# Kernel optimization log

Measured on AMD Instinct MI355X. Metric: run time of the kernel, lower is better.

Reference implementation:

```python
import jax, jax.numpy as jnp
import numpy as np

B, S, D, H = 2, 2048, 2048, 16
HD = D // H
F = 4 * D
EPS = 1e-8


def _layernorm(x, g, b):
    m = jnp.mean(x, axis=-1, keepdims=True)
    v = jnp.mean((x - m) ** 2, axis=-1, keepdims=True)
    return (x - m) / jnp.sqrt(v + EPS) * g + b


def setup_inputs() -> dict:
    key = jax.random.key(0)
    ks = jax.random.split(key, 12)

    def lin(k, fan_in, fan_out):
        # torch Linear init ~ U(-1/sqrt(fan_in), 1/sqrt(fan_in)); stored as [in, out]
        lim = 1.0 / np.sqrt(fan_in)
        kw, kb = jax.random.split(k)
        w = jax.random.uniform(kw, (fan_in, fan_out), jnp.float32, -lim, lim)
        b = jax.random.uniform(kb, (fan_out,), jnp.float32, -lim, lim)
        return w, b

    x = jax.random.normal(ks[0], (B, S, D), jnp.float32)
    wq, bq = lin(ks[1], D, D)
    wk, bk = lin(ks[2], D, D)
    wv, bv = lin(ks[3], D, D)
    wo, bo = lin(ks[4], D, D)
    wu, bu = lin(ks[5], D, F)
    wd, bd = lin(ks[6], F, D)
    g1 = jnp.ones((D,), jnp.float32)
    b1 = jnp.zeros((D,), jnp.float32)
    g2 = jnp.ones((D,), jnp.float32)
    b2 = jnp.zeros((D,), jnp.float32)
    return dict(x=x, wq=wq, bq=bq, wk=wk, bk=bk, wv=wv, bv=bv, wo=wo, bo=bo,
                g1=g1, b1=b1, wu=wu, bu=bu, wd=wd, bd=bd, g2=g2, b2=b2)


def reference(x, wq, bq, wk, bk, wv, bv, wo, bo, g1, b1, wu, bu, wd, bd, g2, b2):
    b, s, d = x.shape
    # QKV projections -> [b, H, s, HD]
    q = (x @ wq + bq).reshape(b, s, H, HD).transpose(0, 2, 1, 3)
    k = (x @ wk + bk).reshape(b, s, H, HD).transpose(0, 2, 1, 3)
    v = (x @ wv + bv).reshape(b, s, H, HD).transpose(0, 2, 1, 3)
    # scaled dot-product with causal mask filled at -1e9 (matches masked_fill)
    scores = jnp.einsum('bhqd,bhkd->bhqk', q, k) / np.sqrt(HD).astype(np.float32)
    causal = jnp.tril(jnp.ones((s, s), bool))
    scores = jnp.where(causal, scores, jnp.float32(-1e9))
    attn = jax.nn.softmax(scores, axis=-1)  # dropout is identity (eval / rate=0)
    o = jnp.einsum('bhqk,bhkd->bhqd', attn, v)
    o = o.transpose(0, 2, 1, 3).reshape(b, s, d)
    o = o @ wo + bo
    x = _layernorm(x + o, g1, b1)
    # FFN with exact (erf) GELU, residual, LN
    h = jax.nn.gelu(x @ wu + bu, approximate=False)
    h = h @ wd + bd
    return _layernorm(x + h, g2, b2)
```

## Files before the change

### kernel.cpp

```cpp
#include <hip/hip_runtime.h>
#include <hip/hip_bf16.h>
#include <math.h>

#define DEV __device__ __forceinline__

typedef __bf16 bf16x8 __attribute__((ext_vector_type(8)));
typedef float f32x4 __attribute__((ext_vector_type(4)));
typedef unsigned short ushort_t;
typedef ushort_t us8 __attribute__((ext_vector_type(8)));
typedef ushort_t us4 __attribute__((ext_vector_type(4)));

DEV float bf2f(ushort_t u) {
    unsigned v = ((unsigned)u) << 16;
    float f; __builtin_memcpy(&f, &v, 4); return f;
}
DEV ushort_t f2bf(float f) {
    unsigned u; __builtin_memcpy(&u, &f, 4);
    u += 0x7fffu + ((u >> 16) & 1);
    return (ushort_t)(u >> 16);
}

DEV void gload16(const void* g, void* l) {
    __builtin_amdgcn_global_load_lds(
        (const __attribute__((address_space(1))) void*)g,
        (__attribute__((address_space(3))) void*)l, 16, 0, 0);
}

__global__ __launch_bounds__(256) void fill_kernel(float* out, long n, float v) {
    long i = (long)blockIdx.x * blockDim.x + threadIdx.x;
    if (i < n) out[i] = v;
}

__global__ __launch_bounds__(256) void cast_bf16_kernel(
    const float* __restrict__ in, ushort_t* __restrict__ out, long n)
{
    long i = ((long)blockIdx.x * blockDim.x + threadIdx.x) * 4;
    if (i >= n) return;
    float4 v = *(const float4*)(in + i);
    us4 o = { f2bf(v.x), f2bf(v.y), f2bf(v.z), f2bf(v.w) };
    *(us4*)(out + i) = o;
}

__global__ __launch_bounds__(256) void transpose_bf16_kernel(
    const float* __restrict__ in, ushort_t* __restrict__ out, int R, int C)
{
    __shared__ float tile[32][33];
    int c0 = blockIdx.x * 32, r0 = blockIdx.y * 32;
    int tx = threadIdx.x & 31, ty = threadIdx.x >> 5;
#pragma unroll
    for (int j = 0; j < 4; ++j) {
        int r = ty + j * 8;
        tile[r][tx] = in[(long)(r0 + r) * C + (c0 + tx)];
    }
    __syncthreads();
#pragma unroll
    for (int j = 0; j < 4; ++j) {
        int r = ty + j * 8;
        out[(long)(c0 + r) * R + (r0 + tx)] = f2bf(tile[tx][r]);
    }
}

__global__ __launch_bounds__(256) void gemm_bt_kernel(
    const ushort_t* __restrict__ A, const ushort_t* __restrict__ Bt,
    const float* __restrict__ bias, ushort_t* __restrict__ C,
    int M, int N, int K, int act)
{
    __shared__ __align__(16) ushort_t lA[128 * 64];
    __shared__ __align__(16) ushort_t lB[128 * 64];
    const int t = threadIdx.x;
    const int w = t >> 6, l = t & 63;
    const int wr = w >> 1, wc = w & 1;
    const long m0 = (long)blockIdx.x * 128;
    const long n0 = (long)blockIdx.y * 128;

    const int sr = l >> 3;
    const int scol = (l & 7) * 16;

    f32x4 acc[4][4];
    f32x4 zf = {0.f, 0.f, 0.f, 0.f};
#pragma unroll
    for (int i = 0; i < 4; ++i)
#pragma unroll
        for (int j = 0; j < 4; ++j) acc[i][j] = zf;

    const char* Ab = (const char*)(A + m0 * K);
    const char* Bb = (const char*)(Bt + n0 * K);
    char* lAc = (char*)lA;
    char* lBc = (char*)lB;

    for (int k0 = 0; k0 < K; k0 += 64) {
        __syncthreads();
#pragma unroll
        for (int c = 0; c < 4; ++c) {
            int row = (w * 4 + c) * 8 + sr;
            int src = scol ^ ((row & 7) << 4);
            gload16(Ab + (long)row * (K * 2) + (long)k0 * 2 + src, lAc + (w * 4 + c) * 1024);
            gload16(Bb + (long)row * (K * 2) + (long)k0 * 2 + src, lBc + (w * 4 + c) * 1024);
        }
        __syncthreads();
#pragma unroll
        for (int ks = 0; ks < 2; ++ks) {
            bf16x8 af[4], bfr[4];
#pragma unroll
            for (int i = 0; i < 4; ++i) {
                int row = wr * 64 + i * 16 + (l & 15);
                int cb = (ks * 64 + (l >> 4) * 16) ^ ((row & 7) << 4);
                af[i] = *(const bf16x8*)(lAc + row * 128 + cb);
            }
#pragma unroll
            for (int j = 0; j < 4; ++j) {
                int row = wc * 64 + j * 16 + (l & 15);
                int cb = (ks * 64 + (l >> 4) * 16) ^ ((row & 7) << 4);
                bfr[j] = *(const bf16x8*)(lBc + row * 128 + cb);
            }
#pragma unroll
            for (int i = 0; i < 4; ++i)
#pragma unroll
                for (int j = 0; j < 4; ++j)
                    acc[i][j] = __builtin_amdgcn_mfma_f32_16x16x32_bf16(af[i], bfr[j], acc[i][j], 0, 0, 0);
        }
    }

#pragma unroll
    for (int j = 0; j < 4; ++j) {
        int col = (int)n0 + wc * 64 + j * 16 + (l & 15);
        float bv = bias[col];
#pragma unroll
        for (int i = 0; i < 4; ++i) {
            long rowb = m0 + wr * 64 + i * 16 + (l >> 4) * 4;
#pragma unroll
            for (int r = 0; r < 4; ++r) {
                float v2 = acc[i][j][r] + bv;
                if (act == 1) v2 = 0.5f * v2 * (1.f + erff(v2 * 0.70710678118654752440f));
                C[(rowb + r) * (long)N + col] = f2bf(v2);
            }
        }
    }
}

__global__ __launch_bounds__(512, 4) void attn_kernel(
    const ushort_t* __restrict__ qkv, ushort_t* __restrict__ o)
{
    __shared__ __align__(16) ushort_t lK[2 * 64 * 128];
    __shared__ __align__(16) ushort_t lVT[128 * 72];
    __shared__ __align__(16) ushort_t lP[8 * 16 * 64];

    const int t = threadIdx.x, w = t >> 6, l = t & 63;
    const int qblk = blockIdx.x, bh = blockIdx.y;
    const int b = bh >> 4, h = bh & 15;
    const int q0 = qblk * 128 + w * 16;
    const long base = (long)b * 2048 * 6144 + (long)h * 128;
    const ushort_t* Kg = qkv + base + 2048;
    const ushort_t* Vg = qkv + base + 4096;
    char* lKc = (char*)lK;

    const ushort_t* qrow = qkv + base + (long)(q0 + (l & 15)) * 6144;
    bf16x8 qf[4];
#pragma unroll
    for (int hb = 0; hb < 4; ++hb)
        qf[hb] = *(const bf16x8*)(qrow + hb * 32 + (l >> 4) * 8);

    f32x4 accO[8];
    f32x4 zf = {0.f, 0.f, 0.f, 0.f};
#pragma unroll
    for (int i = 0; i < 8; ++i) accO[i] = zf;
    float m_r[4] = {-1e30f, -1e30f, -1e30f, -1e30f};
    float l_r[4] = {0.f, 0.f, 0.f, 0.f};

    const int nt = (qblk * 128 + 128) >> 6;
    const float scale = 0.08838834764831845f;

    const int kvp = t & 31;
    const int d0 = (t >> 5) * 8;
    us8 va, vb;

    auto stageK = [&](int kt, int buf) {
#pragma unroll
        for (int i = 0; i < 2; ++i) {
            int c = w * 2 + i;
            int row = c * 4 + (l >> 4);
            int src = ((l & 15) * 16) ^ ((row & 7) << 4);
            gload16((const char*)(Kg + (long)(kt * 64 + row) * 6144) + src,
                    lKc + buf * 16384 + c * 1024);
        }
    };
    auto loadV = [&](int kt) {
        const ushort_t* vr = Vg + (long)(kt * 64 + kvp * 2) * 6144 + d0;
        va = *(const us8*)vr;
        vb = *(const us8*)(vr + 6144);
    };
    auto writeVT = [&]() {
#pragma unroll
        for (int j = 0; j < 8; ++j) {
            unsigned pk = (unsigned)va[j] | ((unsigned)vb[j] << 16);
            *(unsigned*)(lVT + (d0 + j) * 72 + kvp * 2) = pk;
        }
    };

    stageK(0, 0);
    loadV(0);
    asm volatile("s_waitcnt vmcnt(0)" ::: "memory");
    writeVT();
    __syncthreads();

    for (int t0 = 0; t0 < nt; ++t0) {
        const int cur = t0 & 1;
        const bool more = (t0 + 1 < nt);
        if (more) { stageK(t0 + 1, cur ^ 1); loadV(t0 + 1); }

        const int kv0 = t0 * 64;
        if (kv0 <= q0 + 15) {
            f32x4 sc[4];
#pragma unroll
            for (int kvs = 0; kvs < 4; ++kvs) {
                sc[kvs] = zf;
                int row = kvs * 16 + (l & 15);
#pragma unroll
                for (int hb = 0; hb < 4; ++hb) {
                    int cb = (hb * 64 + (l >> 4) * 16) ^ ((row & 7) << 4);
                    bf16x8 kf = *(const bf16x8*)(lKc + cur * 16384 + row * 256 + cb);
                    sc[kvs] = __builtin_amdgcn_mfma_f32_16x16x32_bf16(qf[hb], kf, sc[kvs], 0, 0, 0);
                }
            }
#pragma unroll
            for (int r = 0; r < 4; ++r) {
                int qg = q0 + (l >> 4) * 4 + r;
                float s[4];
#pragma unroll
                for (int kvs = 0; kvs < 4; ++kvs) {
                    s[kvs] = sc[kvs][r] * scale;
                    if (kv0 + kvs * 16 + (l & 15) > qg) s[kvs] = -1e30f;
                }
                float pm = fmaxf(fmaxf(s[0], s[1]), fmaxf(s[2], s[3]));
                pm = fmaxf(pm, __shfl_xor(pm, 1));
                pm = fmaxf(pm, __shfl_xor(pm, 2));
                pm = fmaxf(pm, __shfl_xor(pm, 4));
                pm = fmaxf(pm, __shfl_xor(pm, 8));
                float mn = fmaxf(m_r[r], pm);
                float p[4], ps = 0.f;
#pragma unroll
                for (int kvs = 0; kvs < 4; ++kvs) { p[kvs] = __expf(s[kvs] - mn); ps += p[kvs]; }
                ps += __shfl_xor(ps, 1);
                ps += __shfl_xor(ps, 2);
                ps += __shfl_xor(ps, 4);
                ps += __shfl_xor(ps, 8);
                float alpha = __expf(m_r[r] - mn);
                l_r[r] = l_r[r] * alpha + ps;
                m_r[r] = mn;
#pragma unroll
                for (int tt = 0; tt < 8; ++tt) accO[tt][r] *= alpha;
                int qloc = (l >> 4) * 4 + r;
#pragma unroll
                for (int kvs = 0; kvs < 4; ++kvs)
                    lP[w * 1024 + qloc * 64 + kvs * 16 + (l & 15)] = f2bf(p[kvs]);
            }
            asm volatile("s_waitcnt lgkmcnt(0)" ::: "memory");
#pragma unroll
            for (int ks = 0; ks < 2; ++ks) {
                bf16x8 pf = *(const bf16x8*)(lP + w * 1024 + (l & 15) * 64 + ks * 32 + (l >> 4) * 8);
#pragma unroll
                for (int tt = 0; tt < 8; ++tt) {
                    bf16x8 vf = *(const bf16x8*)(lVT + (tt * 16 + (l & 15)) * 72 + ks * 32 + (l >> 4) * 8);
                    accO[tt] = __builtin_amdgcn_mfma_f32_16x16x32_bf16(pf, vf, accO[tt], 0, 0, 0);
                }
            }
        }

        asm volatile("s_waitcnt vmcnt(0)" ::: "memory");
        __syncthreads();
        if (more) { writeVT(); __syncthreads(); }
    }

    const long obase = (long)b * 2048 * 2048 + (long)h * 128;
#pragma unroll
    for (int r = 0; r < 4; ++r) {
        float inv = 1.f / l_r[r];
        long orow = obase + (long)(q0 + (l >> 4) * 4 + r) * 2048;
#pragma unroll
        for (int tt = 0; tt < 8; ++tt)
            o[orow + tt * 16 + (l & 15)] = f2bf(accO[tt][r] * inv);
    }
}

__global__ __launch_bounds__(256) void ln_kernel(
    const float* xres, const ushort_t* __restrict__ addb,
    const float* __restrict__ g, const float* __restrict__ bb,
    float* outf, ushort_t* __restrict__ outb)
{
    __shared__ float rs[4], rss[4];
    const int row = blockIdx.x, t = threadIdx.x;
    const float* xp = xres + (long)row * 2048 + t * 8;
    const ushort_t* ap = addb + (long)row * 2048 + t * 8;
    float4 a = *(const float4*)xp;
    float4 c = *(const float4*)(xp + 4);
    us8 ad = *(const us8*)ap;
    float v[8];
    v[0] = a.x + bf2f(ad[0]); v[1] = a.y + bf2f(ad[1]);
    v[2] = a.z + bf2f(ad[2]); v[3] = a.w + bf2f(ad[3]);
    v[4] = c.x + bf2f(ad[4]); v[5] = c.y + bf2f(ad[5]);
    v[6] = c.z + bf2f(ad[6]); v[7] = c.w + bf2f(ad[7]);
    float s = 0.f, ss = 0.f;
#pragma unroll
    for (int j = 0; j < 8; ++j) { s += v[j]; ss += v[j] * v[j]; }
#pragma unroll
    for (int off = 32; off > 0; off >>= 1) {
        s += __shfl_down(s, off);
        ss += __shfl_down(ss, off);
    }
    if ((t & 63) == 0) { rs[t >> 6] = s; rss[t >> 6] = ss; }
    __syncthreads();
    float S = rs[0] + rs[1] + rs[2] + rs[3];
    float SS = rss[0] + rss[1] + rss[2] + rss[3];
    float mean = S * (1.f / 2048.f);
    float var = SS * (1.f / 2048.f) - mean * mean;
    float rstd = rsqrtf(var + 1e-8f);
    float of[8];
#pragma unroll
    for (int j = 0; j < 8; ++j) {
        int col = t * 8 + j;
        of[j] = (v[j] - mean) * rstd * g[col] + bb[col];
    }
    float4 o1 = {of[0], of[1], of[2], of[3]};
    float4 o2 = {of[4], of[5], of[6], of[7]};
    float* op = outf + (long)row * 2048 + t * 8;
    *(float4*)op = o1;
    *(float4*)(op + 4) = o2;
    if (outb) {
        us8 ob;
#pragma unroll
        for (int j = 0; j < 8; ++j) ob[j] = f2bf(of[j]);
        *(us8*)(outb + (long)row * 2048 + t * 8) = ob;
    }
}

extern "C" void kernel_launch(void* const* d_in, const int* in_sizes, int n_in,
                              void* d_out, int out_size, void* d_ws, size_t ws_size,
                              hipStream_t stream)
{
    const float* x  = (const float*)d_in[0];
    const float* wq = (const float*)d_in[1];
    const float* bq = (const float*)d_in[2];
    const float* wk = (const float*)d_in[3];
    const float* bk = (const float*)d_in[4];
    const float* wv = (const float*)d_in[5];
    const float* bv = (const float*)d_in[6];
    const float* wo = (const float*)d_in[7];
    const float* bo = (const float*)d_in[8];
    const float* g1 = (const float*)d_in[9];
    const float* b1 = (const float*)d_in[10];
    const float* wu = (const float*)d_in[11];
    const float* bu = (const float*)d_in[12];
    const float* wd = (const float*)d_in[13];
    const float* bd = (const float*)d_in[14];
    const float* g2 = (const float*)d_in[15];
    const float* b2 = (const float*)d_in[16];
    (void)in_sizes; (void)n_in; (void)out_size;

    const size_t MB = 1ull << 20;
    char* wsp = (char*)d_ws;
    char*  slotA = wsp;
    char*  slotB = wsp + 32 * MB;
    char*  slotC = wsp + 48 * MB;
    float* bqkv  = (float*)(wsp + 112 * MB);
    const size_t need = 112 * MB + 32768;
    if (ws_size < need) {
        fill_kernel<<<(8388608 + 255) / 256, 256, 0, stream>>>((float*)d_out, 8388608L, 1e6f);
        return;
    }

    ushort_t* xb   = (ushort_t*)slotB;
    ushort_t* wT   = (ushort_t*)slotA;
    ushort_t* qkvb = (ushort_t*)slotC;
    ushort_t* ab   = (ushort_t*)slotB;
    ushort_t* pb   = (ushort_t*)slotC;
    float*    x1f  = (float*)d_out;
    ushort_t* x1b  = (ushort_t*)slotB;
    ushort_t* hb   = (ushort_t*)slotC;
    ushort_t* db   = (ushort_t*)slotB;

    cast_bf16_kernel<<<8192, 256, 0, stream>>>(x, xb, 8388608L);
    transpose_bf16_kernel<<<dim3(64, 64), 256, 0, stream>>>(wq, wT, 2048, 2048);
    transpose_bf16_kernel<<<dim3(64, 64), 256, 0, stream>>>(wk, wT + 2048ull * 2048, 2048, 2048);
    transpose_bf16_kernel<<<dim3(64, 64), 256, 0, stream>>>(wv, wT + 2ull * 2048 * 2048, 2048, 2048);
    hipMemcpyAsync(bqkv,        bq, 2048 * sizeof(float), hipMemcpyDeviceToDevice, stream);
    hipMemcpyAsync(bqkv + 2048, bk, 2048 * sizeof(float), hipMemcpyDeviceToDevice, stream);
    hipMemcpyAsync(bqkv + 4096, bv, 2048 * sizeof(float), hipMemcpyDeviceToDevice, stream);
    gemm_bt_kernel<<<dim3(32, 48), 256, 0, stream>>>(xb, wT, bqkv, qkvb, 4096, 6144, 2048, 0);
    attn_kernel<<<dim3(16, 32), 512, 0, stream>>>(qkvb, ab);
    transpose_bf16_kernel<<<dim3(64, 64), 256, 0, stream>>>(wo, wT, 2048, 2048);
    gemm_bt_kernel<<<dim3(32, 16), 256, 0, stream>>>(ab, wT, bo, pb, 4096, 2048, 2048, 0);
    ln_kernel<<<4096, 256, 0, stream>>>(x, pb, g1, b1, x1f, x1b);
    transpose_bf16_kernel<<<dim3(256, 64), 256, 0, stream>>>(wu, wT, 2048, 8192);
    gemm_bt_kernel<<<dim3(32, 64), 256, 0, stream>>>(x1b, wT, bu, hb, 4096, 8192, 2048, 1);
    transpose_bf16_kernel<<<dim3(64, 256), 256, 0, stream>>>(wd, wT, 8192, 2048);
    gemm_bt_kernel<<<dim3(32, 16), 256, 0, stream>>>(hb, wT, bd, db, 4096, 2048, 8192, 0);
    ln_kernel<<<4096, 256, 0, stream>>>(x1f, db, g2, b2, (float*)d_out, nullptr);
}
```

Measured before the change: 736.5 us.

## Add 256x256-tile double-buffered GEMM for QKV and FFN-up projections

Introduces a new 512-thread GEMM kernel with 256x256 output tiles, XOR-swizzled LDS, double-buffered global-to-LDS loads interleaved with MFMA phases, and setprio around the MFMA blocks. It replaces the 128x128 GEMM for the two widest projections (QKV and FFN up with GELU). The aim is more operand reuse per byte loaded and overlap of loads with compute. In exchange it uses more registers and LDS, and the grid shrinks to 384 and 512 blocks, which may under-fill the CUs.

Result: slower. 913.2 us (+24.0%).

```diff
diff --git a/kernel.cpp b/kernel.cpp
--- a/kernel.cpp
+++ b/kernel.cpp
@@ -133,6 +133,116 @@
                 float v2 = acc[i][j][r] + bv;
                 if (act == 1) v2 = 0.5f * v2 * (1.f + erff(v2 * 0.70710678118654752440f));
                 C[(rowb + r) * (long)N + col] = f2bf(v2);
+            }
+        }
+    }
+}
+
+__global__ __launch_bounds__(512, 2) void gemm256_kernel(
+    const ushort_t* __restrict__ A, const ushort_t* __restrict__ Bt,
+    const float* __restrict__ bias, ushort_t* __restrict__ C,
+    int M, int N, int K, int act)
+{
+    __shared__ __align__(16) ushort_t lA[2 * 256 * 64];
+    __shared__ __align__(16) ushort_t lB[2 * 256 * 64];
+    const int t = threadIdx.x, l = t & 63;
+    const int w = t >> 6;
+    const int wr = w >> 2, wc = w & 3;
+    const long m0 = (long)blockIdx.x * 256;
+    const long n0 = (long)blockIdx.y * 256;
+    char* lAc = (char*)lA;
+    char* lBc = (char*)lB;
+
+    const int srow = t >> 3;
+    const int scol = (t & 7) * 16;
+
+    f32x4 acc[8][4];
+    f32x4 zf = {0.f, 0.f, 0.f, 0.f};
+#pragma unroll
+    for (int i = 0; i < 8; ++i)
+#pragma unroll
+        for (int j = 0; j < 4; ++j) acc[i][j] = zf;
+
+    const char* Abase = (const char*)A;
+    const char* Bbase = (const char*)Bt;
+
+    auto stageRound = [&](int r, int k0, int buf) {
+        if (r < 4) {
+            int row = r * 64 + srow;
+            int src = scol ^ ((row & 7) << 4);
+            gload16(Abase + ((m0 + row) * (long)K + k0) * 2 + src,
+                    lAc + buf * 32768 + r * 8192 + t * 16);
+        } else {
+            int row = (r - 4) * 64 + srow;
+            int src = scol ^ ((row & 7) << 4);
+            gload16(Bbase + ((n0 + row) * (long)K + k0) * 2 + src,
+                    lBc + buf * 32768 + (r - 4) * 8192 + t * 16);
+        }
+    };
+
+#pragma unroll
+    for (int r = 0; r < 8; ++r) stageRound(r, 0, 0);
+    asm volatile("s_waitcnt vmcnt(0)" ::: "memory");
+    __builtin_amdgcn_s_barrier();
+
+    const int NT = K >> 6;
+    for (int t0 = 0; t0 < NT; ++t0) {
+        const int cur = t0 & 1;
+        const bool more = (t0 + 1 < NT);
+        const int kn = (t0 + 1) << 6;
+#pragma unroll
+        for (int p = 0; p < 4; ++p) {
+            if (more) { stageRound(2 * p, kn, cur ^ 1); stageRound(2 * p + 1, kn, cur ^ 1); }
+            const int qm = p >> 1, qn = p & 1;
+            bf16x8 aF[4][2], bF[2][2];
+#pragma unroll
+            for (int i = 0; i < 4; ++i) {
+                int row = wr * 128 + (qm * 4 + i) * 16 + (l & 15);
+                int rb = cur * 32768 + row * 128;
+                int sw = (row & 7) << 4;
+#pragma unroll
+                for (int ks = 0; ks < 2; ++ks)
+                    aF[i][ks] = *(const bf16x8*)(lAc + rb + ((ks * 64 + (l >> 4) * 16) ^ sw));
+            }
+#pragma unroll
+            for (int j = 0; j < 2; ++j) {
+                int row = wc * 64 + (qn * 2 + j) * 16 + (l & 15);
+                int rb = cur * 32768 + row * 128;
+                int sw = (row & 7) << 4;
+#pragma unroll
+                for (int ks = 0; ks < 2; ++ks)
+                    bF[j][ks] = *(const bf16x8*)(lBc + rb + ((ks * 64 + (l >> 4) * 16) ^ sw));
+            }
+            __builtin_amdgcn_s_setprio(1);
+#pragma unroll
+            for (int i = 0; i < 4; ++i)
+#pragma unroll
+                for (int j = 0; j < 2; ++j)
+#pragma unroll
+                    for (int ks = 0; ks < 2; ++ks)
+                        acc[qm * 4 + i][qn * 2 + j] = __builtin_amdgcn_mfma_f32_16x16x32_bf16(
+                            aF[i][ks], bF[j][ks], acc[qm * 4 + i][qn * 2 + j], 0, 0, 0);
+            __builtin_amdgcn_s_setprio(0);
+            if (p < 3) __builtin_amdgcn_s_barrier();
+        }
+        asm volatile("s_waitcnt lgkmcnt(0)" ::: "memory");
+        asm volatile("s_waitcnt vmcnt(0)" ::: "memory");
+        __builtin_amdgcn_sched_barrier(0);
+        __builtin_amdgcn_s_barrier();
+    }
+
+#pragma unroll
+    for (int ni = 0; ni < 4; ++ni) {
+        int col = (int)n0 + wc * 64 + ni * 16 + (l & 15);
+        float bv = bias[col];
+#pragma unroll
+        for (int mi = 0; mi < 8; ++mi) {
+            long rowb = m0 + wr * 128 + mi * 16 + (l >> 4) * 4;
+#pragma unroll
+            for (int rr = 0; rr < 4; ++rr) {
+                float v2 = acc[mi][ni][rr] + bv;
+                if (act == 1) v2 = 0.5f * v2 * (1.f + erff(v2 * 0.70710678118654752440f));
+                C[(rowb + rr) * (long)N + col] = f2bf(v2);
             }
         }
     }
@@ -385,13 +495,13 @@
     hipMemcpyAsync(bqkv,        bq, 2048 * sizeof(float), hipMemcpyDeviceToDevice, stream);
     hipMemcpyAsync(bqkv + 2048, bk, 2048 * sizeof(float), hipMemcpyDeviceToDevice, stream);
     hipMemcpyAsync(bqkv + 4096, bv, 2048 * sizeof(float), hipMemcpyDeviceToDevice, stream);
-    gemm_bt_kernel<<<dim3(32, 48), 256, 0, stream>>>(xb, wT, bqkv, qkvb, 4096, 6144, 2048, 0);
+    gemm256_kernel<<<dim3(16, 24), 512, 0, stream>>>(xb, wT, bqkv, qkvb, 4096, 6144, 2048, 0);
     attn_kernel<<<dim3(16, 32), 512, 0, stream>>>(qkvb, ab);
     transpose_bf16_kernel<<<dim3(64, 64), 256, 0, stream>>>(wo, wT, 2048, 2048);
     gemm_bt_kernel<<<dim3(32, 16), 256, 0, stream>>>(ab, wT, bo, pb, 4096, 2048, 2048, 0);
     ln_kernel<<<4096, 256, 0, stream>>>(x, pb, g1, b1, x1f, x1b);
     transpose_bf16_kernel<<<dim3(256, 64), 256, 0, stream>>>(wu, wT, 2048, 8192);
-    gemm_bt_kernel<<<dim3(32, 64), 256, 0, stream>>>(x1b, wT, bu, hb, 4096, 8192, 2048, 1);
+    gemm256_kernel<<<dim3(16, 32), 512, 0, stream>>>(x1b, wT, bu, hb, 4096, 8192, 2048, 1);
     transpose_bf16_kernel<<<dim3(64, 256), 256, 0, stream>>>(wd, wT, 8192, 2048);
     gemm_bt_kernel<<<dim3(32, 16), 256, 0, stream>>>(hb, wT, bd, db, 4096, 2048, 8192, 0);
     ln_kernel<<<4096, 256, 0, stream>>>(x1f, db, g2, b2, (float*)d_out, nullptr);
```

## Replace GEMM with triple-buffered 256x128-tile ring kernel and XCD-aware block remap

Applied to the files above, without the earlier changes.

Replaces the single-buffered 128x128 GEMM with a 512-thread kernel computing 256x128 tiles. It keeps a three-slot LDS ring so the global-to-LDS loads for the next two K tiles overlap the MFMA work, using explicit vmcnt waits in place of the two barriers per iteration. It also remaps block IDs across the 8 XCDs to improve L2 locality, and raises wave priority around the MFMA burst. LDS use grows to about 147 KB per block, so only one block fits per CU despite the launch bound asking for two.

Result: slower. 812.7 us (+10.3%).

```diff
diff --git a/kernel.cpp b/kernel.cpp
--- a/kernel.cpp
+++ b/kernel.cpp
@@ -26,6 +26,9 @@
         (__attribute__((address_space(3))) void*)l, 16, 0, 0);
 }
 
+#define WAITV(n) asm volatile("s_waitcnt vmcnt(" #n ")" ::: "memory")
+#define WAITL0()  asm volatile("s_waitcnt lgkmcnt(0)" ::: "memory")
+
 __global__ __launch_bounds__(256) void fill_kernel(float* out, long n, float v) {
     long i = (long)blockIdx.x * blockDim.x + threadIdx.x;
     if (i < n) out[i] = v;
@@ -60,21 +63,29 @@
     }
 }
 
-__global__ __launch_bounds__(256) void gemm_bt_kernel(
+__global__ __launch_bounds__(512, 2) void gemm_ring_kernel(
     const ushort_t* __restrict__ A, const ushort_t* __restrict__ Bt,
     const float* __restrict__ bias, ushort_t* __restrict__ C,
-    int M, int N, int K, int act)
-{
-    __shared__ __align__(16) ushort_t lA[128 * 64];
-    __shared__ __align__(16) ushort_t lB[128 * 64];
-    const int t = threadIdx.x;
-    const int w = t >> 6, l = t & 63;
+    int Mt, int N, int K, int act)
+{
+    __shared__ __align__(16) ushort_t lA[3 * 256 * 64];
+    __shared__ __align__(16) ushort_t lB[3 * 128 * 64];
+    const int t = threadIdx.x, l = t & 63;
+    const int w = t >> 6;
     const int wr = w >> 1, wc = w & 1;
-    const long m0 = (long)blockIdx.x * 128;
-    const long n0 = (long)blockIdx.y * 128;
-
-    const int sr = l >> 3;
-    const int scol = (l & 7) * 16;
+
+    const int nwg = gridDim.x;
+    const int bid = blockIdx.x;
+    const int wg = (bid & 7) * (nwg >> 3) + (bid >> 3);
+    const int bx = wg % Mt, by = wg / Mt;
+    const long m0 = (long)bx * 256;
+    const long n0 = (long)by * 128;
+
+    char* lAc = (char*)lA;
+    char* lBc = (char*)lB;
+
+    const int srow = t >> 3;
+    const int ssrc = ((t & 7) * 16) ^ ((srow & 7) << 4);
 
     f32x4 acc[4][4];
     f32x4 zf = {0.f, 0.f, 0.f, 0.f};
@@ -83,47 +94,78 @@
 #pragma unroll
         for (int j = 0; j < 4; ++j) acc[i][j] = zf;
 
-    const char* Ab = (const char*)(A + m0 * K);
-    const char* Bb = (const char*)(Bt + n0 * K);
-    char* lAc = (char*)lA;
-    char* lBc = (char*)lB;
-
-    for (int k0 = 0; k0 < K; k0 += 64) {
-        __syncthreads();
-#pragma unroll
-        for (int c = 0; c < 4; ++c) {
-            int row = (w * 4 + c) * 8 + sr;
-            int src = scol ^ ((row & 7) << 4);
-            gload16(Ab + (long)row * (K * 2) + (long)k0 * 2 + src, lAc + (w * 4 + c) * 1024);
-            gload16(Bb + (long)row * (K * 2) + (long)k0 * 2 + src, lBc + (w * 4 + c) * 1024);
-        }
-        __syncthreads();
-#pragma unroll
-        for (int ks = 0; ks < 2; ++ks) {
-            bf16x8 af[4], bfr[4];
-#pragma unroll
-            for (int i = 0; i < 4; ++i) {
-                int row = wr * 64 + i * 16 + (l & 15);
-                int cb = (ks * 64 + (l >> 4) * 16) ^ ((row & 7) << 4);
-                af[i] = *(const bf16x8*)(lAc + row * 128 + cb);
-            }
-#pragma unroll
-            for (int j = 0; j < 4; ++j) {
-                int row = wc * 64 + j * 16 + (l & 15);
-                int cb = (ks * 64 + (l >> 4) * 16) ^ ((row & 7) << 4);
-                bfr[j] = *(const bf16x8*)(lBc + row * 128 + cb);
-            }
-#pragma unroll
-            for (int i = 0; i < 4; ++i)
-#pragma unroll
-                for (int j = 0; j < 4; ++j)
-                    acc[i][j] = __builtin_amdgcn_mfma_f32_16x16x32_bf16(af[i], bfr[j], acc[i][j], 0, 0, 0);
-        }
+    const char* Abase = (const char*)A;
+    const char* Bbase = (const char*)Bt;
+
+    auto stageTile = [&](int kt, int slot) {
+        const long kb = (long)kt * 64 * 2;
+#pragma unroll
+        for (int r = 0; r < 4; ++r) {
+            long row = m0 + r * 64 + srow;
+            gload16(Abase + row * (long)K * 2 + kb + ssrc,
+                    lAc + slot * 32768 + r * 8192 + t * 16);
+        }
+#pragma unroll
+        for (int r = 0; r < 2; ++r) {
+            long row = n0 + r * 64 + srow;
+            gload16(Bbase + row * (long)K * 2 + kb + ssrc,
+                    lBc + slot * 16384 + r * 8192 + t * 16);
+        }
+    };
+
+    const int NT = K >> 6;
+    stageTile(0, 0);
+    if (NT > 1) stageTile(1, 1);
+
+    int slot = 0, slot2 = 2;
+    const int rl = l & 15, rh = (l >> 4) * 16;
+    const int swA = ((rl & 7) << 4);
+
+    for (int t0 = 0; t0 < NT; ++t0) {
+        if (t0 + 2 < NT)      { stageTile(t0 + 2, slot2); WAITV(12); }
+        else if (t0 + 1 < NT) { WAITV(6); }
+        else                  { WAITV(0); }
+        __builtin_amdgcn_s_barrier();
+        __builtin_amdgcn_sched_barrier(0);
+
+        bf16x8 aF[4][2], bF[4][2];
+#pragma unroll
+        for (int i = 0; i < 4; ++i) {
+            int row = wr * 64 + i * 16 + rl;
+            int rb = slot * 32768 + row * 128;
+#pragma unroll
+            for (int ks = 0; ks < 2; ++ks)
+                aF[i][ks] = *(const bf16x8*)(lAc + rb + ((ks * 64 + rh) ^ swA));
+        }
+#pragma unroll
+        for (int j = 0; j < 4; ++j) {
+            int row = wc * 64 + j * 16 + rl;
+            int rb = slot * 16384 + row * 128;
+#pragma unroll
+            for (int ks = 0; ks < 2; ++ks)
+                bF[j][ks] = *(const bf16x8*)(lBc + rb + ((ks * 64 + rh) ^ swA));
+        }
+        WAITL0();
+        __builtin_amdgcn_sched_barrier(0);
+        __builtin_amdgcn_s_setprio(1);
+#pragma unroll
+        for (int i = 0; i < 4; ++i)
+#pragma unroll
+            for (int j = 0; j < 4; ++j)
+#pragma unroll
+                for (int ks = 0; ks < 2; ++ks)
+                    acc[i][j] = __builtin_amdgcn_mfma_f32_16x16x32_bf16(
+                        aF[i][ks], bF[j][ks], acc[i][j], 0, 0, 0);
+        __builtin_amdgcn_s_setprio(0);
+        __builtin_amdgcn_s_barrier();
+
+        slot  = (slot  == 2) ? 0 : slot + 1;
+        slot2 = (slot2 == 2) ? 0 : slot2 + 1;
     }
 
 #pragma unroll
     for (int j = 0; j < 4; ++j) {
-        int col = (int)n0 + wc * 64 + j * 16 + (l & 15);
+        int col = (int)n0 + wc * 64 + j * 16 + rl;
         float bv = bias[col];
 #pragma unroll
         for (int i = 0; i < 4; ++i) {
@@ -254,7 +296,7 @@
                 for (int kvs = 0; kvs < 4; ++kvs)
                     lP[w * 1024 + qloc * 64 + kvs * 16 + (l & 15)] = f2bf(p[kvs]);
             }
-            asm volatile("s_waitcnt lgkmcnt(0)" ::: "memory");
+            WAITL0();
 #pragma unroll
             for (int ks = 0; ks < 2; ++ks) {
                 bf16x8 pf = *(const bf16x8*)(lP + w * 1024 + (l & 15) * 64 + ks * 32 + (l >> 4) * 8);
@@ -385,14 +427,14 @@
     hipMemcpyAsync(bqkv,        bq, 2048 * sizeof(float), hipMemcpyDeviceToDevice, stream);
     hipMemcpyAsync(bqkv + 2048, bk, 2048 * sizeof(float), hipMemcpyDeviceToDevice, stream);
     hipMemcpyAsync(bqkv + 4096, bv, 2048 * sizeof(float), hipMemcpyDeviceToDevice, stream);
-    gemm_bt_kernel<<<dim3(32, 48), 256, 0, stream>>>(xb, wT, bqkv, qkvb, 4096, 6144, 2048, 0);
+    gemm_ring_kernel<<<768, 512, 0, stream>>>(xb, wT, bqkv, qkvb, 16, 6144, 2048, 0);
     attn_kernel<<<dim3(16, 32), 512, 0, stream>>>(qkvb, ab);
     transpose_bf16_kernel<<<dim3(64, 64), 256, 0, stream>>>(wo, wT, 2048, 2048);
-    gemm_bt_kernel<<<dim3(32, 16), 256, 0, stream>>>(ab, wT, bo, pb, 4096, 2048, 2048, 0);
+    gemm_ring_kernel<<<256, 512, 0, stream>>>(ab, wT, bo, pb, 16, 2048, 2048, 0);
     ln_kernel<<<4096, 256, 0, stream>>>(x, pb, g1, b1, x1f, x1b);
     transpose_bf16_kernel<<<dim3(256, 64), 256, 0, stream>>>(wu, wT, 2048, 8192);
-    gemm_bt_kernel<<<dim3(32, 64), 256, 0, stream>>>(x1b, wT, bu, hb, 4096, 8192, 2048, 1);
+    gemm_ring_kernel<<<1024, 512, 0, stream>>>(x1b, wT, bu, hb, 16, 8192, 2048, 1);
     transpose_bf16_kernel<<<dim3(64, 256), 256, 0, stream>>>(wd, wT, 8192, 2048);
-    gemm_bt_kernel<<<dim3(32, 16), 256, 0, stream>>>(hb, wT, bd, db, 4096, 2048, 8192, 0);
+    gemm_ring_kernel<<<256, 512, 0, stream>>>(hb, wT, bd, db, 16, 2048, 8192, 0);
     ln_kernel<<<4096, 256, 0, stream>>>(x1f, db, g2, b2, (float*)d_out, nullptr);
 }
```

## Remap GEMM blocks for XCD locality and add K=128 tile GEMM for narrow outputs

Applied to the files above, without the earlier changes.

GEMM launches become 1D grids whose block id is remapped so that consecutive blocks on the same XCD (bid&7 striding) work on neighbouring M tiles. This is meant to improve L2 reuse of shared B tiles. A new GEMM variant with a 128-deep K step and 64 KB of LDS is used for the two N=2048 projections (output proj, down proj). It halves the barrier and load-issue overhead per K step but may lower occupancy.

Result: no change. 739.2 us (+0.4%).

```diff
diff --git a/kernel.cpp b/kernel.cpp
--- a/kernel.cpp
+++ b/kernel.cpp
@@ -63,15 +63,17 @@
 __global__ __launch_bounds__(256) void gemm_bt_kernel(
     const ushort_t* __restrict__ A, const ushort_t* __restrict__ Bt,
     const float* __restrict__ bias, ushort_t* __restrict__ C,
-    int M, int N, int K, int act)
+    int Mt, int N, int K, int act)
 {
     __shared__ __align__(16) ushort_t lA[128 * 64];
     __shared__ __align__(16) ushort_t lB[128 * 64];
     const int t = threadIdx.x;
     const int w = t >> 6, l = t & 63;
     const int wr = w >> 1, wc = w & 1;
-    const long m0 = (long)blockIdx.x * 128;
-    const long n0 = (long)blockIdx.y * 128;
+    const int nwg = gridDim.x, bid = blockIdx.x;
+    const int id = (bid & 7) * (nwg >> 3) + (bid >> 3);
+    const long m0 = (long)(id % Mt) * 128;
+    const long n0 = (long)(id / Mt) * 128;
 
     const int sr = l >> 3;
     const int scol = (l & 7) * 16;
@@ -112,6 +114,85 @@
                 int row = wc * 64 + j * 16 + (l & 15);
                 int cb = (ks * 64 + (l >> 4) * 16) ^ ((row & 7) << 4);
                 bfr[j] = *(const bf16x8*)(lBc + row * 128 + cb);
+            }
+#pragma unroll
+            for (int i = 0; i < 4; ++i)
+#pragma unroll
+                for (int j = 0; j < 4; ++j)
+                    acc[i][j] = __builtin_amdgcn_mfma_f32_16x16x32_bf16(af[i], bfr[j], acc[i][j], 0, 0, 0);
+        }
+    }
+
+#pragma unroll
+    for (int j = 0; j < 4; ++j) {
+        int col = (int)n0 + wc * 64 + j * 16 + (l & 15);
+        float bv = bias[col];
+#pragma unroll
+        for (int i = 0; i < 4; ++i) {
+            long rowb = m0 + wr * 64 + i * 16 + (l >> 4) * 4;
+#pragma unroll
+            for (int r = 0; r < 4; ++r) {
+                float v2 = acc[i][j][r] + bv;
+                if (act == 1) v2 = 0.5f * v2 * (1.f + erff(v2 * 0.70710678118654752440f));
+                C[(rowb + r) * (long)N + col] = f2bf(v2);
+            }
+        }
+    }
+}
+
+__global__ __launch_bounds__(256) void gemm_bt128_kernel(
+    const ushort_t* __restrict__ A, const ushort_t* __restrict__ Bt,
+    const float* __restrict__ bias, ushort_t* __restrict__ C,
+    int Mt, int N, int K, int act)
+{
+    __shared__ __align__(16) ushort_t lA[128 * 128];
+    __shared__ __align__(16) ushort_t lB[128 * 128];
+    const int t = threadIdx.x;
+    const int w = t >> 6, l = t & 63;
+    const int wr = w >> 1, wc = w & 1;
+    const int nwg = gridDim.x, bid = blockIdx.x;
+    const int id = (bid & 7) * (nwg >> 3) + (bid >> 3);
+    const long m0 = (long)(id % Mt) * 128;
+    const long n0 = (long)(id / Mt) * 128;
+
+    const int srow = t >> 4;
+    const int ssrc = ((t & 15) * 16) ^ ((srow & 7) << 4);
+
+    f32x4 acc[4][4];
+    f32x4 zf = {0.f, 0.f, 0.f, 0.f};
+#pragma unroll
+    for (int i = 0; i < 4; ++i)
+#pragma unroll
+        for (int j = 0; j < 4; ++j) acc[i][j] = zf;
+
+    const char* Ab = (const char*)(A + m0 * K);
+    const char* Bb = (const char*)(Bt + n0 * K);
+    char* lAc = (char*)lA;
+    char* lBc = (char*)lB;
+
+    for (int k0 = 0; k0 < K; k0 += 128) {
+        __syncthreads();
+#pragma unroll
+        for (int r = 0; r < 8; ++r) {
+            int row = r * 16 + srow;
+            gload16(Ab + (long)row * (K * 2) + (long)k0 * 2 + ssrc, lAc + r * 4096 + t * 16);
+            gload16(Bb + (long)row * (K * 2) + (long)k0 * 2 + ssrc, lBc + r * 4096 + t * 16);
+        }
+        __syncthreads();
+#pragma unroll
+        for (int ks = 0; ks < 4; ++ks) {
+            bf16x8 af[4], bfr[4];
+#pragma unroll
+            for (int i = 0; i < 4; ++i) {
+                int row = wr * 64 + i * 16 + (l & 15);
+                int cb = (ks * 64 + (l >> 4) * 16) ^ ((row & 7) << 4);
+                af[i] = *(const bf16x8*)(lAc + row * 256 + cb);
+            }
+#pragma unroll
+            for (int j = 0; j < 4; ++j) {
+                int row = wc * 64 + j * 16 + (l & 15);
+                int cb = (ks * 64 + (l >> 4) * 16) ^ ((row & 7) << 4);
+                bfr[j] = *(const bf16x8*)(lBc + row * 256 + cb);
             }
 #pragma unroll
             for (int i = 0; i < 4; ++i)
@@ -385,14 +466,14 @@
     hipMemcpyAsync(bqkv,        bq, 2048 * sizeof(float), hipMemcpyDeviceToDevice, stream);
     hipMemcpyAsync(bqkv + 2048, bk, 2048 * sizeof(float), hipMemcpyDeviceToDevice, stream);
     hipMemcpyAsync(bqkv + 4096, bv, 2048 * sizeof(float), hipMemcpyDeviceToDevice, stream);
-    gemm_bt_kernel<<<dim3(32, 48), 256, 0, stream>>>(xb, wT, bqkv, qkvb, 4096, 6144, 2048, 0);
+    gemm_bt_kernel<<<1536, 256, 0, stream>>>(xb, wT, bqkv, qkvb, 32, 6144, 2048, 0);
     attn_kernel<<<dim3(16, 32), 512, 0, stream>>>(qkvb, ab);
     transpose_bf16_kernel<<<dim3(64, 64), 256, 0, stream>>>(wo, wT, 2048, 2048);
-    gemm_bt_kernel<<<dim3(32, 16), 256, 0, stream>>>(ab, wT, bo, pb, 4096, 2048, 2048, 0);
+    gemm_bt128_kernel<<<512, 256, 0, stream>>>(ab, wT, bo, pb, 32, 2048, 2048, 0);
     ln_kernel<<<4096, 256, 0, stream>>>(x, pb, g1, b1, x1f, x1b);
     transpose_bf16_kernel<<<dim3(256, 64), 256, 0, stream>>>(wu, wT, 2048, 8192);
-    gemm_bt_kernel<<<dim3(32, 64), 256, 0, stream>>>(x1b, wT, bu, hb, 4096, 8192, 2048, 1);
+    gemm_bt_kernel<<<2048, 256, 0, stream>>>(x1b, wT, bu, hb, 32, 8192, 2048, 1);
     transpose_bf16_kernel<<<dim3(64, 256), 256, 0, stream>>>(wd, wT, 8192, 2048);
-    gemm_bt_kernel<<<dim3(32, 16), 256, 0, stream>>>(hb, wT, bd, db, 4096, 2048, 8192, 0);
+    gemm_bt128_kernel<<<512, 256, 0, stream>>>(hb, wT, bd, db, 32, 2048, 8192, 0);
     ln_kernel<<<4096, 256, 0, stream>>>(x1f, db, g2, b2, (float*)d_out, nullptr);
 }
```
